# Kernel tuning notes

Measured on AMD Instinct MI355X. Metric: run time of the kernel, lower is better.

Reference implementation:

```python
import jax, jax.numpy as jnp
import numpy as np

GAMMA = 0.99
LAM = 0.95
CLIP = 0.2
VALUE_COEFF = 0.5
ENTROPY_COEFF = 0.01
T = 500_000
S = 128
A = 16


def _mlp(x, W1, b1, W2, b2, W3, b3):
    h = jax.nn.relu(x @ W1 + b1)
    h = jax.nn.relu(h @ W2 + b2)
    return h @ W3 + b3


def setup_inputs() -> dict:
    key = jax.random.key(0)
    ks = jax.random.split(key, 12)
    states = jax.random.normal(ks[0], (T, S), dtype=jnp.float32)
    next_states = jax.random.normal(ks[1], (T, S), dtype=jnp.float32)
    rewards = jax.random.normal(ks[2], (T,), dtype=jnp.float32)
    dones = (jax.random.uniform(ks[3], (T,)) < 0.01).astype(jnp.float32)
    actions = jax.random.randint(ks[4], (T,), 0, A)
    # old log-probs of taken actions (valid log-probabilities)
    old_logp = jnp.log(jax.random.uniform(ks[5], (T,), minval=1e-3, maxval=1.0))

    def lin(k, fan_in, fan_out):
        lim = 1.0 / np.sqrt(fan_in)
        return jax.random.uniform(k, (fan_in, fan_out), minval=-lim, maxval=lim, dtype=jnp.float32)

    return {
        'states': states, 'next_states': next_states, 'rewards': rewards,
        'dones': dones, 'actions': actions, 'old_logp': old_logp,
        'aW1': lin(ks[6], S, 64), 'ab1': jnp.zeros((64,), jnp.float32),
        'aW2': lin(ks[7], 64, 64), 'ab2': jnp.zeros((64,), jnp.float32),
        'aW3': lin(ks[8], 64, A), 'ab3': jnp.zeros((A,), jnp.float32),
        'cW1': lin(ks[9], S, 64), 'cb1': jnp.zeros((64,), jnp.float32),
        'cW2': lin(ks[10], 64, 64), 'cb2': jnp.zeros((64,), jnp.float32),
        'cW3': lin(ks[11], 64, 1), 'cb3': jnp.zeros((1,), jnp.float32),
    }


def reference(states, next_states, rewards, dones, actions, old_logp,
              aW1, ab1, aW2, ab2, aW3, ab3,
              cW1, cb1, cW2, cb2, cW3, cb3):
    # ---- critic values and TD deltas ----
    values = _mlp(states, cW1, cb1, cW2, cb2, cW3, cb3)[:, 0]        # [T]
    next_values = _mlp(next_states, cW1, cb1, cW2, cb2, cW3, cb3)[:, 0]
    not_done = 1.0 - dones
    deltas = rewards + GAMMA * next_values * not_done - values       # [T]

    # ---- GAE: reverse-time linear recurrence a_t = c_t * a_{t+1} + d_t ----
    coef = GAMMA * LAM * not_done

    def step(carry, cd):
        c, d = cd
        a = c * carry + d
        return a, a

    _, advantages = jax.lax.scan(step, jnp.float32(0.0), (coef, deltas), reverse=True)
    returns = advantages + values
    adv_n = (advantages - advantages.mean()) / (jnp.std(advantages, ddof=1) + 1e-8)

    # ---- actor: clipped surrogate ----
    probs = jax.nn.softmax(_mlp(states, aW1, ab1, aW2, ab2, aW3, ab3), axis=-1)  # [T, A]
    logp = jnp.log(jnp.take_along_axis(probs, actions[:, None], axis=1))[:, 0]   # [T]
    ratios = jnp.exp(logp - old_logp)
    surr1 = ratios * adv_n
    surr2 = jnp.clip(ratios, 1.0 - CLIP, 1.0 + CLIP) * adv_n
    actor_loss = -jnp.minimum(surr1, surr2).mean()

    # ---- critic MSE loss ----
    critic_loss = jnp.mean((values - returns) ** 2)

    # ---- entropy bonus ----
    entropy_loss = jnp.mean(-jnp.sum(probs * jnp.log(probs + 1e-8), axis=-1))

    total_loss = actor_loss + VALUE_COEFF * critic_loss - ENTROPY_COEFF * entropy_loss
    return jnp.stack([total_loss, actor_loss, critic_loss, entropy_loss])
```

## Files before the change

kernel.cpp:

```cpp
#include <hip/hip_runtime.h>
#include <hip/hip_bf16.h>

#define T_N 500000
#define NTILE 31250
#define NBLK 512
#define NWAVES (NBLK * 4)
#define NCHUNK 4096
#define CHUNKL 128
#define NPART 1024

typedef __attribute__((ext_vector_type(8))) short short8v;
typedef __attribute__((ext_vector_type(4))) float float4v;

__device__ __forceinline__ short f2bf(float f) {
    __hip_bfloat16 b = __float2bfloat16(f);
    return *reinterpret_cast<short*>(&b);
}
__device__ __forceinline__ float bf2f(short s) {
    return __uint_as_float(((unsigned)(unsigned short)s) << 16);
}

__device__ __forceinline__ short8v cvt8(const float4 a, const float4 b) {
    short8v r;
    r[0] = f2bf(a.x); r[1] = f2bf(a.y); r[2] = f2bf(a.z); r[3] = f2bf(a.w);
    r[4] = f2bf(b.x); r[5] = f2bf(b.y); r[6] = f2bf(b.z); r[7] = f2bf(b.w);
    return r;
}

#define FC1 0
#define FA1 16
#define FC2 32
#define FA2 40
#define FA3 48
#define NFRAG 50

__global__ __launch_bounds__(64) void k_pack(
    const float* __restrict__ cW1, const float* __restrict__ aW1,
    const float* __restrict__ cW2, const float* __restrict__ aW2,
    const float* __restrict__ aW3, short8v* __restrict__ packed)
{
    const int f = blockIdx.x, l = threadIdx.x;
    const int g = l >> 4, col = l & 15;
    const float* W; int s, c, ncol;
    if (f < FA1)      { W = cW1; s = f >> 2;         c = f & 3;         ncol = 64; }
    else if (f < FC2) { W = aW1; s = (f - FA1) >> 2; c = (f - FA1) & 3; ncol = 64; }
    else if (f < FA2) { W = cW2; s = (f - FC2) >> 2; c = (f - FC2) & 3; ncol = 64; }
    else if (f < FA3) { W = aW2; s = (f - FA2) >> 2; c = (f - FA2) & 3; ncol = 64; }
    else              { W = aW3; s = f - FA3;        c = 0;             ncol = 16; }
    short8v frag;
    #pragma unroll
    for (int j = 0; j < 8; ++j) {
        int k = s * 32 + g * 8 + j;
        frag[j] = f2bf(W[k * ncol + c * 16 + col]);
    }
    packed[f * 64 + l] = frag;
}

__device__ __forceinline__ void store_h(short (*hb)[68], const float4v* acc, int g, int q) {
    #pragma unroll
    for (int c = 0; c < 4; ++c)
        #pragma unroll
        for (int r = 0; r < 4; ++r)
            hb[g * 4 + r][c * 16 + q] = f2bf(fmaxf(acc[c][r], 0.f));
}

__global__ __launch_bounds__(256) void k_mlp(
    const float* __restrict__ states, const float* __restrict__ next_states,
    const short8v* __restrict__ pk,
    const float* __restrict__ cb1, const float* __restrict__ ab1,
    const float* __restrict__ cb2, const float* __restrict__ ab2,
    const float* __restrict__ ab3,
    const float* __restrict__ cW3, const float* __restrict__ cb3,
    float* __restrict__ v_o, float* __restrict__ nv_o,
    short* __restrict__ logit_o)
{
    __shared__ __align__(16) short8v spk[NFRAG * 64];
    __shared__ __align__(16) short hlds[4][2][16][68];
    const int wv = threadIdx.x >> 6, l = threadIdx.x & 63;
    const int g = l >> 4, q = l & 15;
    short (*h0)[68] = hlds[wv][0];
    short (*h1)[68] = hlds[wv][1];

    for (int i = threadIdx.x; i < NFRAG * 64; i += 256) spk[i] = pk[i];
    __syncthreads();

    int tile = blockIdx.x * 4 + wv;
    if (tile >= NTILE) return;

    float bc1[4], bc2[4], ba1[4], ba2[4], w3[4];
    #pragma unroll
    for (int c = 0; c < 4; ++c) {
        bc1[c] = cb1[c * 16 + q];
        bc2[c] = cb2[c * 16 + q];
        ba1[c] = ab1[c * 16 + q];
        ba2[c] = ab2[c * 16 + q];
        w3[c]  = cW3[c * 16 + q];
    }
    const float ab3q = ab3[q];
    const float cb3v = cb3[0];

    float4 rs[8], rn[8];
    {
        const float* xs = states + ((long long)tile * 16 + q) * 128 + g * 8;
        const float* xn = next_states + ((long long)tile * 16 + q) * 128 + g * 8;
        #pragma unroll
        for (int s = 0; s < 4; ++s) {
            rs[2 * s]     = *reinterpret_cast<const float4*>(xs + s * 32);
            rs[2 * s + 1] = *reinterpret_cast<const float4*>(xs + s * 32 + 4);
            rn[2 * s]     = *reinterpret_cast<const float4*>(xn + s * 32);
            rn[2 * s + 1] = *reinterpret_cast<const float4*>(xn + s * 32 + 4);
        }
    }

    while (true) {
        const int next = tile + NWAVES;
        const long long r0 = (long long)tile * 16;

        short8v sa[4], na[4];
        #pragma unroll
        for (int s = 0; s < 4; ++s) {
            sa[s] = cvt8(rs[2 * s], rs[2 * s + 1]);
            na[s] = cvt8(rn[2 * s], rn[2 * s + 1]);
        }

        if (next < NTILE) {
            const float* xs = states + ((long long)next * 16 + q) * 128 + g * 8;
            const float* xn = next_states + ((long long)next * 16 + q) * 128 + g * 8;
            #pragma unroll
            for (int s = 0; s < 4; ++s) {
                rs[2 * s]     = *reinterpret_cast<const float4*>(xs + s * 32);
                rs[2 * s + 1] = *reinterpret_cast<const float4*>(xs + s * 32 + 4);
                rn[2 * s]     = *reinterpret_cast<const float4*>(xn + s * 32);
                rn[2 * s + 1] = *reinterpret_cast<const float4*>(xn + s * 32 + 4);
            }
        }

        float4v accC[4], accN[4];
        #pragma unroll
        for (int c = 0; c < 4; ++c) {
            accC[c] = (float4v){bc1[c], bc1[c], bc1[c], bc1[c]};
            accN[c] = accC[c];
        }
        #pragma unroll
        for (int s = 0; s < 4; ++s) {
            #pragma unroll
            for (int c = 0; c < 4; ++c) {
                short8v w = spk[(FC1 + s * 4 + c) * 64 + l];
                accC[c] = __builtin_amdgcn_mfma_f32_16x16x32_bf16(sa[s], w, accC[c], 0, 0, 0);
                accN[c] = __builtin_amdgcn_mfma_f32_16x16x32_bf16(na[s], w, accN[c], 0, 0, 0);
            }
        }
        store_h(h0, accC, g, q);
        store_h(h1, accN, g, q);

        float4v c2C[4], c2N[4];
        #pragma unroll
        for (int c = 0; c < 4; ++c) {
            c2C[c] = (float4v){bc2[c], bc2[c], bc2[c], bc2[c]};
            c2N[c] = c2C[c];
        }
        #pragma unroll
        for (int s = 0; s < 2; ++s) {
            short8v aC = *reinterpret_cast<const short8v*>(&h0[q][s * 32 + g * 8]);
            short8v aN = *reinterpret_cast<const short8v*>(&h1[q][s * 32 + g * 8]);
            #pragma unroll
            for (int c = 0; c < 4; ++c) {
                short8v w = spk[(FC2 + s * 4 + c) * 64 + l];
                c2C[c] = __builtin_amdgcn_mfma_f32_16x16x32_bf16(aC, w, c2C[c], 0, 0, 0);
                c2N[c] = __builtin_amdgcn_mfma_f32_16x16x32_bf16(aN, w, c2N[c], 0, 0, 0);
            }
        }
        float vr[4] = {0.f, 0.f, 0.f, 0.f}, nr[4] = {0.f, 0.f, 0.f, 0.f};
        #pragma unroll
        for (int c = 0; c < 4; ++c) {
            #pragma unroll
            for (int r = 0; r < 4; ++r) {
                vr[r] = fmaf(fmaxf(c2C[c][r], 0.f), w3[c], vr[r]);
                nr[r] = fmaf(fmaxf(c2N[c][r], 0.f), w3[c], nr[r]);
            }
        }
        #pragma unroll
        for (int o = 1; o < 16; o <<= 1)
            #pragma unroll
            for (int r = 0; r < 4; ++r) {
                vr[r] += __shfl_xor(vr[r], o);
                nr[r] += __shfl_xor(nr[r], o);
            }
        if (q == 0) {
            float4 tv, tn;
            tv.x = vr[0] + cb3v; tv.y = vr[1] + cb3v; tv.z = vr[2] + cb3v; tv.w = vr[3] + cb3v;
            tn.x = nr[0] + cb3v; tn.y = nr[1] + cb3v; tn.z = nr[2] + cb3v; tn.w = nr[3] + cb3v;
            *reinterpret_cast<float4*>(&v_o[r0 + g * 4])  = tv;
            *reinterpret_cast<float4*>(&nv_o[r0 + g * 4]) = tn;
        }

        float4v aA[4];
        #pragma unroll
        for (int c = 0; c < 4; ++c) aA[c] = (float4v){ba1[c], ba1[c], ba1[c], ba1[c]};
        #pragma unroll
        for (int s = 0; s < 4; ++s)
            #pragma unroll
            for (int c = 0; c < 4; ++c)
                aA[c] = __builtin_amdgcn_mfma_f32_16x16x32_bf16(sa[s], spk[(FA1 + s * 4 + c) * 64 + l], aA[c], 0, 0, 0);
        store_h(h0, aA, g, q);

        float4v a2[4];
        #pragma unroll
        for (int c = 0; c < 4; ++c) a2[c] = (float4v){ba2[c], ba2[c], ba2[c], ba2[c]};
        #pragma unroll
        for (int s = 0; s < 2; ++s) {
            short8v aa = *reinterpret_cast<const short8v*>(&h0[q][s * 32 + g * 8]);
            #pragma unroll
            for (int c = 0; c < 4; ++c)
                a2[c] = __builtin_amdgcn_mfma_f32_16x16x32_bf16(aa, spk[(FA2 + s * 4 + c) * 64 + l], a2[c], 0, 0, 0);
        }
        store_h(h1, a2, g, q);

        float4v a3 = (float4v){ab3q, ab3q, ab3q, ab3q};
        #pragma unroll
        for (int s = 0; s < 2; ++s) {
            short8v aa = *reinterpret_cast<const short8v*>(&h1[q][s * 32 + g * 8]);
            a3 = __builtin_amdgcn_mfma_f32_16x16x32_bf16(aa, spk[(FA3 + s) * 64 + l], a3, 0, 0, 0);
        }
        #pragma unroll
        for (int r = 0; r < 4; ++r)
            logit_o[(r0 + g * 4 + r) * 16 + q] = f2bf(a3[r]);

        if (next >= NTILE) break;
        tile = next;
    }
}

__device__ __forceinline__ void dc_elem(float v, float nv, float rw, float dn,
                                        float& d, float& c) {
    float nd = 1.f - dn;
    d = fmaf(0.99f * nd, nv, rw) - v;
    c = (0.99f * 0.95f) * nd;
}

__global__ __launch_bounds__(256) void k_gae_chunk(
    const float* __restrict__ v_i, const float* __restrict__ nv_i,
    const float* __restrict__ rewards, const float* __restrict__ dones,
    float* __restrict__ P, float* __restrict__ Q)
{
    const int c = blockIdx.x * 256 + threadIdx.x;
    const long long lo = (long long)c * CHUNKL;
    float p = 1.f, a = 0.f;
    if (lo < T_N) {
        const int n = (int)((T_N - lo < CHUNKL) ? (T_N - lo) : CHUNKL);
        for (int j = (n >> 2) - 1; j >= 0; --j) {
            float4 vv = *reinterpret_cast<const float4*>(&v_i[lo + 4 * j]);
            float4 nn = *reinterpret_cast<const float4*>(&nv_i[lo + 4 * j]);
            float4 rw = *reinterpret_cast<const float4*>(&rewards[lo + 4 * j]);
            float4 dn = *reinterpret_cast<const float4*>(&dones[lo + 4 * j]);
            float d0, c0, d1, c1, d2, c2, d3, c3;
            dc_elem(vv.x, nn.x, rw.x, dn.x, d0, c0);
            dc_elem(vv.y, nn.y, rw.y, dn.y, d1, c1);
            dc_elem(vv.z, nn.z, rw.z, dn.z, d2, c2);
            dc_elem(vv.w, nn.w, rw.w, dn.w, d3, c3);
            a = fmaf(c3, a, d3);
            a = fmaf(c2, a, d2);
            a = fmaf(c1, a, d1);
            a = fmaf(c0, a, d0);
            p *= c0 * c1 * c2 * c3;
        }
    }
    P[c] = p; Q[c] = a;
}

__global__ __launch_bounds__(1024) void k_gae_scan(
    const float* __restrict__ P, const float* __restrict__ Q,
    float* __restrict__ carry)
{
    __shared__ float sp[1024], sq[1024];
    const int t = threadIdx.x, b = t * 4;
    float p = P[b + 3], q = Q[b + 3];
    #pragma unroll
    for (int c = 2; c >= 0; --c) {
        float pc = P[b + c], qc = Q[b + c];
        q = fmaf(pc, q, qc);
        p = pc * p;
    }
    sp[t] = p; sq[t] = q;
    __syncthreads();
    for (int d = 1; d < 1024; d <<= 1) {
        float pp = sp[t], qq = sq[t];
        float p2 = 1.f, q2 = 0.f;
        const bool has = (t + d) < 1024;
        if (has) { p2 = sp[t + d]; q2 = sq[t + d]; }
        __syncthreads();
        if (has) { sp[t] = pp * p2; sq[t] = fmaf(pp, q2, qq); }
        __syncthreads();
    }
    float x = (t + 1 < 1024) ? sq[t + 1] : 0.f;
    #pragma unroll
    for (int c = 3; c >= 0; --c) {
        carry[b + c] = x;
        x = fmaf(P[b + c], x, Q[b + c]);
    }
}

__global__ __launch_bounds__(256) void k_gae_apply(
    const float* __restrict__ v_i, const float* __restrict__ nv_i,
    const float* __restrict__ rewards, const float* __restrict__ dones,
    const float* __restrict__ carry, float* __restrict__ adv,
    float* __restrict__ part)
{
    const int c = blockIdx.x * 256 + threadIdx.x;
    const long long lo = (long long)c * CHUNKL;
    float s = 0.f, s2 = 0.f;
    if (lo < T_N) {
        const int n = (int)((T_N - lo < CHUNKL) ? (T_N - lo) : CHUNKL);
        float a = carry[c];
        for (int j = (n >> 2) - 1; j >= 0; --j) {
            float4 vv = *reinterpret_cast<const float4*>(&v_i[lo + 4 * j]);
            float4 nn = *reinterpret_cast<const float4*>(&nv_i[lo + 4 * j]);
            float4 rw = *reinterpret_cast<const float4*>(&rewards[lo + 4 * j]);
            float4 dn = *reinterpret_cast<const float4*>(&dones[lo + 4 * j]);
            float d0, c0, d1, c1, d2, c2, d3, c3;
            dc_elem(vv.x, nn.x, rw.x, dn.x, d0, c0);
            dc_elem(vv.y, nn.y, rw.y, dn.y, d1, c1);
            dc_elem(vv.z, nn.z, rw.z, dn.z, d2, c2);
            dc_elem(vv.w, nn.w, rw.w, dn.w, d3, c3);
            float a3 = fmaf(c3, a, d3);
            float a2v = fmaf(c2, a3, d2);
            float a1 = fmaf(c1, a2v, d1);
            float a0 = fmaf(c0, a1, d0);
            float4 o; o.x = a0; o.y = a1; o.z = a2v; o.w = a3;
            *reinterpret_cast<float4*>(&adv[lo + 4 * j]) = o;
            a = a0;
            s += a0 + a1 + a2v + a3;
            s2 += a0 * a0 + a1 * a1 + a2v * a2v + a3 * a3;
        }
    }
    #pragma unroll
    for (int o = 32; o > 0; o >>= 1) { s += __shfl_down(s, o); s2 += __shfl_down(s2, o); }
    __shared__ float l0[4], l1[4];
    const int wv = threadIdx.x >> 6, ln = threadIdx.x & 63;
    if (ln == 0) { l0[wv] = s; l1[wv] = s2; }
    __syncthreads();
    if (threadIdx.x == 0) {
        part[blockIdx.x * 2]     = l0[0] + l0[1] + l0[2] + l0[3];
        part[blockIdx.x * 2 + 1] = l1[0] + l1[1] + l1[2] + l1[3];
    }
}

__global__ __launch_bounds__(256) void k_actor(
    const float* __restrict__ adv, const short* __restrict__ logits,
    const float* __restrict__ old_logp, const int* __restrict__ actions,
    const float* __restrict__ part, float* __restrict__ part4)
{
    __shared__ float st[2];
    if (threadIdx.x == 0) {
        float S = 0.f, S2 = 0.f;
        #pragma unroll
        for (int i = 0; i < 16; ++i) { S += part[2 * i]; S2 += part[2 * i + 1]; }
        const float Tf = (float)T_N;
        float mean = S / Tf;
        float var = (S2 - S * S / Tf) / (Tf - 1.f);
        st[0] = mean;
        st[1] = 1.f / (sqrtf(fmaxf(var, 0.f)) + 1e-8f);
    }
    __syncthreads();
    const float mean = st[0], isd = st[1];
    float sm = 0.f, sent = 0.f;
    for (long long i = (long long)blockIdx.x * 256 + threadIdx.x; i < T_N;
         i += (long long)gridDim.x * 256) {
        const short8v* lp = reinterpret_cast<const short8v*>(logits) + i * 2;
        short8v lo0 = lp[0], lo1 = lp[1];
        float lg[16];
        #pragma unroll
        for (int j = 0; j < 8; ++j) { lg[j] = bf2f(lo0[j]); lg[8 + j] = bf2f(lo1[j]); }
        float m = lg[0];
        #pragma unroll
        for (int a = 1; a < 16; ++a) m = fmaxf(m, lg[a]);
        float se = 0.f, tt = 0.f;
        #pragma unroll
        for (int a = 0; a < 16; ++a) {
            float e = __expf(lg[a] - m);
            se += e;
            tt = fmaf(e, lg[a], tt);
        }
        float ls = __logf(se);
        float ent = m + ls - tt / se;
        const int act = actions[i];
        float lsel = lg[0];
        #pragma unroll
        for (int a = 1; a < 16; ++a) lsel = (a == act) ? lg[a] : lsel;
        float logp = lsel - m - ls;
        float rt = __expf(logp - old_logp[i]);
        float an = (adv[i] - mean) * isd;
        sm += fminf(rt * an, fminf(fmaxf(rt, 0.8f), 1.2f) * an);
        sent += ent;
    }
    #pragma unroll
    for (int o = 32; o > 0; o >>= 1) { sm += __shfl_down(sm, o); sent += __shfl_down(sent, o); }
    __shared__ float l0[4], l1[4];
    const int wv = threadIdx.x >> 6, ln = threadIdx.x & 63;
    if (ln == 0) { l0[wv] = sm; l1[wv] = sent; }
    __syncthreads();
    if (threadIdx.x == 0) {
        part4[blockIdx.x * 2]     = l0[0] + l0[1] + l0[2] + l0[3];
        part4[blockIdx.x * 2 + 1] = l1[0] + l1[1] + l1[2] + l1[3];
    }
}

__global__ __launch_bounds__(1024) void k_final(
    const float* __restrict__ part4, const float* __restrict__ part,
    float* __restrict__ out)
{
    const int t = threadIdx.x;
    float sm = part4[t * 2], se = part4[t * 2 + 1];
    #pragma unroll
    for (int o = 32; o > 0; o >>= 1) { sm += __shfl_down(sm, o); se += __shfl_down(se, o); }
    __shared__ float l0[16], l1[16];
    const int wv = t >> 6, ln = t & 63;
    if (ln == 0) { l0[wv] = sm; l1[wv] = se; }
    __syncthreads();
    if (t == 0) {
        float SM = 0.f, SE = 0.f;
        #pragma unroll
        for (int i = 0; i < 16; ++i) { SM += l0[i]; SE += l1[i]; }
        float S2 = 0.f;
        #pragma unroll
        for (int i = 0; i < 16; ++i) S2 += part[2 * i + 1];
        const float Tf = (float)T_N;
        float actor_loss = -SM / Tf;
        float ent_loss = SE / Tf;
        float critic_loss = S2 / Tf;
        float total = actor_loss + 0.5f * critic_loss - 0.01f * ent_loss;
        out[0] = total; out[1] = actor_loss; out[2] = critic_loss; out[3] = ent_loss;
    }
}

extern "C" void kernel_launch(void* const* d_in, const int* in_sizes, int n_in,
                              void* d_out, int out_size, void* d_ws, size_t ws_size,
                              hipStream_t stream) {
    (void)in_sizes; (void)n_in; (void)out_size; (void)ws_size;
    const float* states      = (const float*)d_in[0];
    const float* next_states = (const float*)d_in[1];
    const float* rewards     = (const float*)d_in[2];
    const float* dones       = (const float*)d_in[3];
    const int*   actions     = (const int*)d_in[4];
    const float* old_logp    = (const float*)d_in[5];
    const float* aW1 = (const float*)d_in[6];  const float* ab1 = (const float*)d_in[7];
    const float* aW2 = (const float*)d_in[8];  const float* ab2 = (const float*)d_in[9];
    const float* aW3 = (const float*)d_in[10]; const float* ab3 = (const float*)d_in[11];
    const float* cW1 = (const float*)d_in[12]; const float* cb1 = (const float*)d_in[13];
    const float* cW2 = (const float*)d_in[14]; const float* cb2 = (const float*)d_in[15];
    const float* cW3 = (const float*)d_in[16]; const float* cb3 = (const float*)d_in[17];
    float* out = (float*)d_out;

    short* logits = (short*)d_ws;
    float* fbase = (float*)(logits + (size_t)T_N * 16);
    float* v_ws  = fbase;
    float* nv_ws = fbase + (size_t)T_N;
    float* adv   = fbase + 2 * (size_t)T_N;
    float* P     = fbase + 3 * (size_t)T_N;
    float* Q     = P + NCHUNK;
    float* carry = Q + NCHUNK;
    float* part  = carry + NCHUNK;
    float* part4 = part + 32;
    short8v* packed = (short8v*)(part4 + 2048);

    k_pack<<<NFRAG, 64, 0, stream>>>(cW1, aW1, cW2, aW2, aW3, packed);
    k_mlp<<<NBLK, 256, 0, stream>>>(
        states, next_states, packed,
        cb1, ab1, cb2, ab2, ab3, cW3, cb3, v_ws, nv_ws, logits);
    k_gae_chunk<<<NCHUNK / 256, 256, 0, stream>>>(v_ws, nv_ws, rewards, dones, P, Q);
    k_gae_scan<<<1, 1024, 0, stream>>>(P, Q, carry);
    k_gae_apply<<<NCHUNK / 256, 256, 0, stream>>>(v_ws, nv_ws, rewards, dones, carry, adv, part);
    k_actor<<<NPART, 256, 0, stream>>>(adv, logits, old_logp, actions, part, part4);
    k_final<<<1, 1024, 0, stream>>>(part4, part, out);
}
```

Before: 209.2 us.

## Stage MLP input tiles via async global-to-LDS loads with double buffering

Input rows for states and next_states are now loaded with global_load_lds straight into XOR-swizzled per-wave LDS buffers, two tiles ahead, replacing register prefetch. The packed weight fragments are no longer copied to LDS; MFMA operands are read from global memory, relying on cache. Grid size is halved to fit the larger LDS footprint. The goal is deeper memory-latency hiding on the streaming input at the cost of lower occupancy and more global weight loads inside the inner loop.

After: 258.9 us. 1.24x slower.

```diff
diff --git a/kernel.cpp b/kernel.cpp
--- a/kernel.cpp
+++ b/kernel.cpp
@@ -3,7 +3,7 @@
 
 #define T_N 500000
 #define NTILE 31250
-#define NBLK 512
+#define NBLK 256
 #define NWAVES (NBLK * 4)
 #define NCHUNK 4096
 #define CHUNKL 128
@@ -64,6 +64,23 @@
             hb[g * 4 + r][c * 16 + q] = f2bf(fmaxf(acc[c][r], 0.f));
 }
 
+__device__ __forceinline__ void stage16(const char* __restrict__ sb,
+                                        const char* __restrict__ nb,
+                                        char* ls, char* ln, int l)
+{
+    #pragma unroll
+    for (int k = 0; k < 8; ++k) {
+        const int rl = 2 * k + (l >> 5);
+        const int so = ((l & 31) * 16) ^ ((rl & 7) << 4);
+        __builtin_amdgcn_global_load_lds(
+            (const __attribute__((address_space(1))) void*)(sb + rl * 512 + so),
+            (__attribute__((address_space(3))) void*)(ls + k * 1024), 16, 0, 0);
+        __builtin_amdgcn_global_load_lds(
+            (const __attribute__((address_space(1))) void*)(nb + rl * 512 + so),
+            (__attribute__((address_space(3))) void*)(ln + k * 1024), 16, 0, 0);
+    }
+}
+
 __global__ __launch_bounds__(256) void k_mlp(
     const float* __restrict__ states, const float* __restrict__ next_states,
     const short8v* __restrict__ pk,
@@ -74,18 +91,12 @@
     float* __restrict__ v_o, float* __restrict__ nv_o,
     short* __restrict__ logit_o)
 {
-    __shared__ __align__(16) short8v spk[NFRAG * 64];
+    __shared__ __align__(16) char xlds[4][2][2][8192];
     __shared__ __align__(16) short hlds[4][2][16][68];
     const int wv = threadIdx.x >> 6, l = threadIdx.x & 63;
     const int g = l >> 4, q = l & 15;
     short (*h0)[68] = hlds[wv][0];
     short (*h1)[68] = hlds[wv][1];
-
-    for (int i = threadIdx.x; i < NFRAG * 64; i += 256) spk[i] = pk[i];
-    __syncthreads();
-
-    int tile = blockIdx.x * 4 + wv;
-    if (tile >= NTILE) return;
 
     float bc1[4], bc2[4], ba1[4], ba2[4], w3[4];
     #pragma unroll
@@ -99,41 +110,43 @@
     const float ab3q = ab3[q];
     const float cb3v = cb3[0];
 
-    float4 rs[8], rn[8];
-    {
-        const float* xs = states + ((long long)tile * 16 + q) * 128 + g * 8;
-        const float* xn = next_states + ((long long)tile * 16 + q) * 128 + g * 8;
+    const int wid = blockIdx.x * 4 + wv;
+    long long t = wid;
+    const long long S = NWAVES;
+
+    stage16((const char*)states + t * 8192, (const char*)next_states + t * 8192,
+            &xlds[wv][0][0][0], &xlds[wv][0][1][0], l);
+    if (t + S < NTILE)
+        stage16((const char*)states + (t + S) * 8192, (const char*)next_states + (t + S) * 8192,
+                &xlds[wv][1][0][0], &xlds[wv][1][1][0], l);
+    int cur = 0;
+
+    const int swz = (q & 7) << 4;
+    const int qb = q * 512;
+
+    for (; t < NTILE; t += S, cur ^= 1) {
+        const long long r0 = t * 16;
+
+        asm volatile("s_waitcnt vmcnt(0)" ::: "memory");
+
+        const char* xs = &xlds[wv][cur][0][0];
+        const char* xn = &xlds[wv][cur][1][0];
+        short8v sa[4], na[4];
         #pragma unroll
         for (int s = 0; s < 4; ++s) {
-            rs[2 * s]     = *reinterpret_cast<const float4*>(xs + s * 32);
-            rs[2 * s + 1] = *reinterpret_cast<const float4*>(xs + s * 32 + 4);
-            rn[2 * s]     = *reinterpret_cast<const float4*>(xn + s * 32);
-            rn[2 * s + 1] = *reinterpret_cast<const float4*>(xn + s * 32 + 4);
-        }
-    }
-
-    while (true) {
-        const int next = tile + NWAVES;
-        const long long r0 = (long long)tile * 16;
-
-        short8v sa[4], na[4];
-        #pragma unroll
-        for (int s = 0; s < 4; ++s) {
-            sa[s] = cvt8(rs[2 * s], rs[2 * s + 1]);
-            na[s] = cvt8(rn[2 * s], rn[2 * s + 1]);
-        }
-
-        if (next < NTILE) {
-            const float* xs = states + ((long long)next * 16 + q) * 128 + g * 8;
-            const float* xn = next_states + ((long long)next * 16 + q) * 128 + g * 8;
-            #pragma unroll
-            for (int s = 0; s < 4; ++s) {
-                rs[2 * s]     = *reinterpret_cast<const float4*>(xs + s * 32);
-                rs[2 * s + 1] = *reinterpret_cast<const float4*>(xs + s * 32 + 4);
-                rn[2 * s]     = *reinterpret_cast<const float4*>(xn + s * 32);
-                rn[2 * s + 1] = *reinterpret_cast<const float4*>(xn + s * 32 + 4);
-            }
-        }
+            const int p = s * 128 + g * 32;
+            float4 fa = *reinterpret_cast<const float4*>(xs + qb + (p ^ swz));
+            float4 fb = *reinterpret_cast<const float4*>(xs + qb + ((p + 16) ^ swz));
+            sa[s] = cvt8(fa, fb);
+            float4 ga = *reinterpret_cast<const float4*>(xn + qb + (p ^ swz));
+            float4 gb = *reinterpret_cast<const float4*>(xn + qb + ((p + 16) ^ swz));
+            na[s] = cvt8(ga, gb);
+        }
+        asm volatile("s_waitcnt lgkmcnt(0)" ::: "memory");
+        if (t + 2 * S < NTILE)
+            stage16((const char*)states + (t + 2 * S) * 8192,
+                    (const char*)next_states + (t + 2 * S) * 8192,
+                    &xlds[wv][cur][0][0], &xlds[wv][cur][1][0], l);
 
         float4v accC[4], accN[4];
         #pragma unroll
@@ -145,7 +158,7 @@
         for (int s = 0; s < 4; ++s) {
             #pragma unroll
             for (int c = 0; c < 4; ++c) {
-                short8v w = spk[(FC1 + s * 4 + c) * 64 + l];
+                short8v w = pk[(FC1 + s * 4 + c) * 64 + l];
                 accC[c] = __builtin_amdgcn_mfma_f32_16x16x32_bf16(sa[s], w, accC[c], 0, 0, 0);
                 accN[c] = __builtin_amdgcn_mfma_f32_16x16x32_bf16(na[s], w, accN[c], 0, 0, 0);
             }
@@ -165,7 +178,7 @@
             short8v aN = *reinterpret_cast<const short8v*>(&h1[q][s * 32 + g * 8]);
             #pragma unroll
             for (int c = 0; c < 4; ++c) {
-                short8v w = spk[(FC2 + s * 4 + c) * 64 + l];
+                short8v w = pk[(FC2 + s * 4 + c) * 64 + l];
                 c2C[c] = __builtin_amdgcn_mfma_f32_16x16x32_bf16(aC, w, c2C[c], 0, 0, 0);
                 c2N[c] = __builtin_amdgcn_mfma_f32_16x16x32_bf16(aN, w, c2N[c], 0, 0, 0);
             }
@@ -201,7 +214,7 @@
         for (int s = 0; s < 4; ++s)
             #pragma unroll
             for (int c = 0; c < 4; ++c)
-                aA[c] = __builtin_amdgcn_mfma_f32_16x16x32_bf16(sa[s], spk[(FA1 + s * 4 + c) * 64 + l], aA[c], 0, 0, 0);
+                aA[c] = __builtin_amdgcn_mfma_f32_16x16x32_bf16(sa[s], pk[(FA1 + s * 4 + c) * 64 + l], aA[c], 0, 0, 0);
         store_h(h0, aA, g, q);
 
         float4v a2[4];
@@ -212,7 +225,7 @@
             short8v aa = *reinterpret_cast<const short8v*>(&h0[q][s * 32 + g * 8]);
             #pragma unroll
             for (int c = 0; c < 4; ++c)
-                a2[c] = __builtin_amdgcn_mfma_f32_16x16x32_bf16(aa, spk[(FA2 + s * 4 + c) * 64 + l], a2[c], 0, 0, 0);
+                a2[c] = __builtin_amdgcn_mfma_f32_16x16x32_bf16(aa, pk[(FA2 + s * 4 + c) * 64 + l], a2[c], 0, 0, 0);
         }
         store_h(h1, a2, g, q);
 
@@ -220,14 +233,11 @@
         #pragma unroll
         for (int s = 0; s < 2; ++s) {
             short8v aa = *reinterpret_cast<const short8v*>(&h1[q][s * 32 + g * 8]);
-            a3 = __builtin_amdgcn_mfma_f32_16x16x32_bf16(aa, spk[(FA3 + s) * 64 + l], a3, 0, 0, 0);
+            a3 = __builtin_amdgcn_mfma_f32_16x16x32_bf16(aa, pk[(FA3 + s) * 64 + l], a3, 0, 0, 0);
         }
         #pragma unroll
         for (int r = 0; r < 4; ++r)
             logit_o[(r0 + g * 4 + r) * 16 + q] = f2bf(a3[r]);
-
-        if (next >= NTILE) break;
-        tile = next;
     }
 }
 
```
